# Performance work log

Measured on AMD Instinct MI355X. Metric: run time of the kernel, lower is better.

## Reference

```python
import jax, jax.numpy as jnp
import numpy as np

B, S, D, H = 8, 1024, 1024, 16
DH = D // H


def setup_inputs() -> dict:
    key = jax.random.key(0)
    ks = jax.random.split(key, 7)
    scale = 1.0 / np.sqrt(DH)
    return {
        "sequences": jax.random.normal(ks[0], (B, S, D), dtype=jnp.float32),
        "Wq": jax.random.uniform(ks[1], (H, DH, DH), jnp.float32, -scale, scale),
        "bq": jax.random.uniform(ks[2], (H, DH), jnp.float32, -scale, scale),
        "Wk": jax.random.uniform(ks[3], (H, DH, DH), jnp.float32, -scale, scale),
        "bk": jax.random.uniform(ks[4], (H, DH), jnp.float32, -scale, scale),
        "Wv": jax.random.uniform(ks[5], (H, DH, DH), jnp.float32, -scale, scale),
        "bv": jax.random.uniform(ks[6], (H, DH), jnp.float32, -scale, scale),
    }


def reference(sequences, Wq, bq, Wk, bk, Wv, bv):
    # split channels into heads: [B,S,H,DH]
    x = sequences.reshape(B, S, H, DH)
    # per-head linear maps (torch Linear: y = x @ W.T + b)
    q = jnp.einsum("bshd,hed->bshe", x, Wq) + bq  # [B,S,H,DH]
    k = jnp.einsum("bshd,hed->bshe", x, Wk) + bk
    v = jnp.einsum("bshd,hed->bshe", x, Wv) + bv
    scores = jnp.einsum("bshd,bthd->bhst", q, k) / jnp.sqrt(jnp.asarray(DH, x.dtype))
    attn = jax.nn.softmax(scores, axis=-1)  # [B,H,S,S]
    out = jnp.einsum("bhst,bthd->bshd", attn, v)  # [B,S,H,DH]
    return out.reshape(B, S, D)
```

## Files before the change

### kernel.cpp

```cpp
#include <hip/hip_runtime.h>
#include <hip/hip_bf16.h>


constexpr int NB = 8, NS = 1024, ND = 1024, NH = 16, NDH = 64;

typedef __bf16 bf16x8 __attribute__((ext_vector_type(8)));
typedef short bf16x4s __attribute__((ext_vector_type(4)));
typedef float f32x4 __attribute__((ext_vector_type(4)));

__device__ __forceinline__ f32x4 mfma16(bf16x8 a, bf16x8 b, f32x4 c) {
  return __builtin_amdgcn_mfma_f32_16x16x32_bf16(a, b, c, 0, 0, 0);
}

__device__ __forceinline__ f32x4 mfma16k16(bf16x4s a, bf16x4s b, f32x4 c) {
#if __has_builtin(__builtin_amdgcn_mfma_f32_16x16x16bf16_1k)
  return __builtin_amdgcn_mfma_f32_16x16x16bf16_1k(a, b, c, 0, 0, 0);
#else
  f32x4 d;
  asm("v_mfma_f32_16x16x16_bf16 %0, %1, %2, %3"
      : "=v"(d) : "v"(a), "v"(b), "v"(c));
  return d;
#endif
}

__device__ __forceinline__ float fast_exp2(float x) {
#if __has_builtin(__builtin_amdgcn_exp2f)
  return __builtin_amdgcn_exp2f(x);
#else
  return __builtin_exp2f(x);
#endif
}

__device__ __forceinline__ bf16x8 cvt2bf8(float4 lo, float4 hi) {
  bf16x8 r;
  r[0] = (__bf16)lo.x; r[1] = (__bf16)lo.y; r[2] = (__bf16)lo.z; r[3] = (__bf16)lo.w;
  r[4] = (__bf16)hi.x; r[5] = (__bf16)hi.y; r[6] = (__bf16)hi.z; r[7] = (__bf16)hi.w;
  return r;
}

__device__ __forceinline__ void gload16(const __hip_bfloat16* g, __hip_bfloat16* l) {
  __builtin_amdgcn_global_load_lds(
      (const __attribute__((address_space(1))) void*)g,
      (__attribute__((address_space(3))) void*)l, 16, 0, 0);
}

__device__ __forceinline__ unsigned pack_bf16(float hi, float lo) {
  unsigned uh = __builtin_bit_cast(unsigned, hi) + 0x8000u;
  unsigned ul = __builtin_bit_cast(unsigned, lo) + 0x8000u;
  return __builtin_amdgcn_perm(uh, ul, 0x07060302u);
}

__global__ __launch_bounds__(256) void qkv_proj_kernel(
    const float* __restrict__ x,
    const float* __restrict__ Wq, const float* __restrict__ bq,
    const float* __restrict__ Wk, const float* __restrict__ bk,
    const float* __restrict__ Wv, const float* __restrict__ bv,
    __hip_bfloat16* __restrict__ Qo, __hip_bfloat16* __restrict__ Ko,
    __hip_bfloat16* __restrict__ Vt) {
  __shared__ __align__(16) __hip_bfloat16 Wlds[3][NDH][72];
  const int tid = threadIdx.x;
  const int wave = tid >> 6, lane = tid & 63;
  const int m = lane & 15, quad = lane >> 4;
  const int h = blockIdx.x & (NH - 1);
  const int sblk = blockIdx.x >> 4;

  const float* Ws[3] = {Wq + h * 4096, Wk + h * 4096, Wv + h * 4096};
#pragma unroll
  for (int mt = 0; mt < 3; mt++) {
#pragma unroll
    for (int p = 0; p < 4; p++) {
      int idx = (p * 256 + tid) * 4;
      float4 v = *(const float4*)(Ws[mt] + idx);
      __align__(8) __hip_bfloat16 t4[4] = {
          __float2bfloat16(v.x), __float2bfloat16(v.y),
          __float2bfloat16(v.z), __float2bfloat16(v.w)};
      *(uint2*)&Wlds[mt][idx >> 6][idx & 63] = *(const uint2*)t4;
    }
  }
  __syncthreads();

  float bq4[4][4], bk4[4][4], bvv[4];
#pragma unroll
  for (int nt = 0; nt < 4; nt++) {
    float4 a = *(const float4*)(bq + h * 64 + nt * 16 + quad * 4);
    float4 c = *(const float4*)(bk + h * 64 + nt * 16 + quad * 4);
    bq4[nt][0] = a.x; bq4[nt][1] = a.y; bq4[nt][2] = a.z; bq4[nt][3] = a.w;
    bk4[nt][0] = c.x; bk4[nt][1] = c.y; bk4[nt][2] = c.z; bk4[nt][3] = c.w;
    bvv[nt] = bv[h * 64 + nt * 16 + m];
  }

  const int rowbase = sblk * 256 + wave * 64;
  bf16x8 Xf[4][2];
#pragma unroll
  for (int st = 0; st < 4; st++) {
    const float* xp = x + (size_t)(rowbase + st * 16 + m) * ND + h * NDH + quad * 8;
#pragma unroll
    for (int c = 0; c < 2; c++) {
      float4 lo = *(const float4*)(xp + c * 32);
      float4 hi = *(const float4*)(xp + c * 32 + 4);
      Xf[st][c] = cvt2bf8(lo, hi);
    }
  }

  const int b = rowbase >> 10;
  const int s0 = rowbase & 1023;
  const float qscale = 0.18033688011112042f;

#pragma unroll
  for (int mt = 0; mt < 3; mt++) {
#pragma unroll
    for (int nt = 0; nt < 4; nt++) {
      bf16x8 w0 = *(const bf16x8*)&Wlds[mt][nt * 16 + m][quad * 8];
      bf16x8 w1 = *(const bf16x8*)&Wlds[mt][nt * 16 + m][32 + quad * 8];
#pragma unroll
      for (int st = 0; st < 4; st++) {
        f32x4 acc = {0.f, 0.f, 0.f, 0.f};
        if (mt < 2) {
          acc = mfma16(w0, Xf[st][0], acc);
          acc = mfma16(w1, Xf[st][1], acc);
          const int srow = s0 + st * 16 + m;
          __align__(8) __hip_bfloat16 t4[4];
          if (mt == 0) {
#pragma unroll
            for (int r = 0; r < 4; r++)
              t4[r] = __float2bfloat16((acc[r] + bq4[nt][r]) * qscale);
            *(uint2*)(Qo + ((size_t)(b * NH + h) * NS + srow) * NDH +
                      nt * 16 + quad * 4) = *(const uint2*)t4;
          } else {
#pragma unroll
            for (int r = 0; r < 4; r++)
              t4[r] = __float2bfloat16(acc[r] + bk4[nt][r]);
            *(uint2*)(Ko + ((size_t)(b * NH + h) * NS + srow) * NDH +
                      nt * 16 + quad * 4) = *(const uint2*)t4;
          }
        } else {
          acc = mfma16(Xf[st][0], w0, acc);
          acc = mfma16(Xf[st][1], w1, acc);
          __align__(8) __hip_bfloat16 t4[4];
#pragma unroll
          for (int r = 0; r < 4; r++) t4[r] = __float2bfloat16(acc[r] + bvv[nt]);
          *(uint2*)(Vt + ((size_t)(b * NH + h) * NDH + nt * 16 + m) * NS + s0 +
                    st * 16 + quad * 4) = *(const uint2*)t4;
        }
      }
    }
  }
}

__global__ __launch_bounds__(256, 2) void attn_kernel(
    const __hip_bfloat16* __restrict__ Q,
    const __hip_bfloat16* __restrict__ K,
    const __hip_bfloat16* __restrict__ Vt,
    float* __restrict__ out) {
  __shared__ __align__(16) __hip_bfloat16 Kt[2][64][64];
  __shared__ __align__(16) __hip_bfloat16 Vl[2][64][64];

  const int tid = threadIdx.x;
  const int wave = tid >> 6, lane = tid & 63;
  const int m = lane & 15, quad = lane >> 4;

  const int xcd = blockIdx.x & 7;
  const int j = blockIdx.x >> 3;
  const int bh = xcd * 16 + (j & 15);
  const int qblk = j >> 4;
  const int qbase = qblk * 256 + wave * 64;

  const __hip_bfloat16* Qp = Q + (size_t)bh * NS * NDH;
  const __hip_bfloat16* Kp = K + (size_t)bh * NS * NDH;
  const __hip_bfloat16* Vp = Vt + (size_t)bh * NDH * NS;

  bf16x8 Bq[4][2];
#pragma unroll
  for (int g = 0; g < 4; g++)
#pragma unroll
    for (int c = 0; c < 2; c++)
      Bq[g][c] = *(const bf16x8*)(Qp + (size_t)(qbase + g * 16 + m) * NDH +
                                  c * 32 + quad * 8);

  f32x4 accO[4][4];
  f32x4 lsum[4];
#pragma unroll
  for (int g = 0; g < 4; g++) {
    lsum[g] = (f32x4){0.f, 0.f, 0.f, 0.f};
#pragma unroll
    for (int nt = 0; nt < 4; nt++) accO[g][nt] = (f32x4){0.f, 0.f, 0.f, 0.f};
  }
  const bf16x4s ones4 = {0x3F80, 0x3F80, 0x3F80, 0x3F80};

  const int r8 = lane >> 3;
  const int cs = (lane & 7) ^ r8;
  const int pc = quad ^ (m & 7);
  int voffs[4];
#pragma unroll
  for (int s = 0; s < 4; s++)
    voffs[s] = (((2 * s) | (quad >> 1)) ^ (m & 7)) * 8 + (quad & 1) * 4;

#define STAGE(buf, tb)                                                        \
  {                                                                           \
    _Pragma("unroll") for (int p = 0; p < 2; p++) {                           \
      const int row = wave * 16 + p * 8;                                      \
      gload16(Kp + (size_t)((tb) * 64 + row + r8) * NDH + cs * 8,             \
              &Kt[buf][row][0]);                                              \
      gload16(Vp + (size_t)(row + r8) * NS + (tb) * 64 + cs * 8,              \
              &Vl[buf][row][0]);                                              \
    }                                                                         \
  }

  STAGE(0, 0);

  for (int tb = 0; tb < NS / 64; tb++) {
    const int cur = tb & 1;
    __syncthreads();
    if (tb + 1 < NS / 64) STAGE(cur ^ 1, tb + 1);

    bf16x8 kf[4][2];
#pragma unroll
    for (int nt = 0; nt < 4; nt++) {
      kf[nt][0] = *(const bf16x8*)&Kt[cur][nt * 16 + m][pc * 8];
      kf[nt][1] = *(const bf16x8*)&Kt[cur][nt * 16 + m][(pc ^ 4) * 8];
    }
    bf16x4s vf[4][4];
#pragma unroll
    for (int nt = 0; nt < 4; nt++)
#pragma unroll
      for (int s = 0; s < 4; s++)
        vf[nt][s] = __builtin_bit_cast(
            bf16x4s, *(const uint2*)&Vl[cur][nt * 16 + m][voffs[s]]);

#pragma unroll
    for (int g = 0; g < 4; g++) {
      f32x4 sc[4];
#pragma unroll
      for (int s = 0; s < 4; s++) {
        f32x4 a = {0.f, 0.f, 0.f, 0.f};
        a = mfma16(kf[s][0], Bq[g][0], a);
        a = mfma16(kf[s][1], Bq[g][1], a);
        sc[s] = a;
      }
      bf16x4s Pa[4];
#pragma unroll
      for (int s = 0; s < 4; s++) {
        float e0 = fast_exp2(sc[s][0]);
        float e1 = fast_exp2(sc[s][1]);
        float e2 = fast_exp2(sc[s][2]);
        float e3 = fast_exp2(sc[s][3]);
        uint2 w;
        w.x = pack_bf16(e1, e0);
        w.y = pack_bf16(e3, e2);
        Pa[s] = __builtin_bit_cast(bf16x4s, w);
      }
#pragma unroll
      for (int s = 0; s < 4; s++) lsum[g] = mfma16k16(Pa[s], ones4, lsum[g]);
#pragma unroll
      for (int nt = 0; nt < 4; nt++)
#pragma unroll
        for (int s = 0; s < 4; s++)
          accO[g][nt] = mfma16k16(Pa[s], vf[nt][s], accO[g][nt]);
    }
  }
#undef STAGE

  const int b = bh >> 4, h = bh & (NH - 1);
#pragma unroll
  for (int g = 0; g < 4; g++) {
#pragma unroll
    for (int r = 0; r < 4; r++) {
      float inv = 1.0f / lsum[g][r];
      int srow = qbase + g * 16 + quad * 4 + r;
      float* op = out + (size_t)(b * NS + srow) * ND + h * NDH;
#pragma unroll
      for (int nt = 0; nt < 4; nt++) op[nt * 16 + m] = accO[g][nt][r] * inv;
    }
  }
}

extern "C" void kernel_launch(void* const* d_in, const int* in_sizes, int n_in,
                              void* d_out, int out_size, void* d_ws, size_t ws_size,
                              hipStream_t stream) {
  const float* x  = (const float*)d_in[0];
  const float* Wq = (const float*)d_in[1];
  const float* bq = (const float*)d_in[2];
  const float* Wk = (const float*)d_in[3];
  const float* bk = (const float*)d_in[4];
  const float* Wv = (const float*)d_in[5];
  const float* bv = (const float*)d_in[6];
  float* out = (float*)d_out;

  const size_t elems = (size_t)NB * NH * NS * NDH;
  __hip_bfloat16* Qw = (__hip_bfloat16*)d_ws;
  __hip_bfloat16* Kw = Qw + elems;
  __hip_bfloat16* Vw = Kw + elems;

  qkv_proj_kernel<<<512, 256, 0, stream>>>(x, Wq, bq, Wk, bk, Wv, bv, Qw, Kw, Vw);
  attn_kernel<<<512, 256, 0, stream>>>(Qw, Kw, Vw, out);
}
```

Measured before the change: 149.6 us.

## Halve query rows per attention block to raise occupancy and grid size

Each attention wave now handles 32 query rows instead of 64, and each block 128 instead of 256. The grid doubles to 1024 blocks and the launch bound rises to 4 blocks per CU. The inner loop is reordered so score MFMAs, exp and packing happen per key subtile, and V fragments are loaded per output subtile, which cuts live registers. In exchange, each K/V tile staged in shared memory is reused by half as many queries, so shared-memory and L2 traffic double, and barrier overhead per unit of MFMA work grows.

```diff
diff --git a/kernel.cpp b/kernel.cpp
--- a/kernel.cpp
+++ b/kernel.cpp
@@ -147,7 +147,7 @@
   }
 }
 
-__global__ __launch_bounds__(256, 2) void attn_kernel(
+__global__ __launch_bounds__(256, 4) void attn_kernel(
     const __hip_bfloat16* __restrict__ Q,
     const __hip_bfloat16* __restrict__ K,
     const __hip_bfloat16* __restrict__ Vt,
@@ -163,24 +163,24 @@
   const int j = blockIdx.x >> 3;
   const int bh = xcd * 16 + (j & 15);
   const int qblk = j >> 4;
-  const int qbase = qblk * 256 + wave * 64;
+  const int qbase = qblk * 128 + wave * 32;
 
   const __hip_bfloat16* Qp = Q + (size_t)bh * NS * NDH;
   const __hip_bfloat16* Kp = K + (size_t)bh * NS * NDH;
   const __hip_bfloat16* Vp = Vt + (size_t)bh * NDH * NS;
 
-  bf16x8 Bq[4][2];
-#pragma unroll
-  for (int g = 0; g < 4; g++)
+  bf16x8 Bq[2][2];
+#pragma unroll
+  for (int g = 0; g < 2; g++)
 #pragma unroll
     for (int c = 0; c < 2; c++)
       Bq[g][c] = *(const bf16x8*)(Qp + (size_t)(qbase + g * 16 + m) * NDH +
                                   c * 32 + quad * 8);
 
-  f32x4 accO[4][4];
-  f32x4 lsum[4];
-#pragma unroll
-  for (int g = 0; g < 4; g++) {
+  f32x4 accO[2][4];
+  f32x4 lsum[2];
+#pragma unroll
+  for (int g = 0; g < 2; g++) {
     lsum[g] = (f32x4){0.f, 0.f, 0.f, 0.f};
 #pragma unroll
     for (int nt = 0; nt < 4; nt++) accO[g][nt] = (f32x4){0.f, 0.f, 0.f, 0.f};
@@ -213,56 +213,45 @@
     __syncthreads();
     if (tb + 1 < NS / 64) STAGE(cur ^ 1, tb + 1);
 
-    bf16x8 kf[4][2];
+    bf16x4s Pa[2][4];
+#pragma unroll
+    for (int s = 0; s < 4; s++) {
+      bf16x8 k0 = *(const bf16x8*)&Kt[cur][s * 16 + m][pc * 8];
+      bf16x8 k1 = *(const bf16x8*)&Kt[cur][s * 16 + m][(pc ^ 4) * 8];
+#pragma unroll
+      for (int g = 0; g < 2; g++) {
+        f32x4 a = {0.f, 0.f, 0.f, 0.f};
+        a = mfma16(k0, Bq[g][0], a);
+        a = mfma16(k1, Bq[g][1], a);
+        uint2 w;
+        w.x = pack_bf16(fast_exp2(a[1]), fast_exp2(a[0]));
+        w.y = pack_bf16(fast_exp2(a[3]), fast_exp2(a[2]));
+        Pa[g][s] = __builtin_bit_cast(bf16x4s, w);
+      }
+    }
+#pragma unroll
+    for (int g = 0; g < 2; g++)
+#pragma unroll
+      for (int s = 0; s < 4; s++) lsum[g] = mfma16k16(Pa[g][s], ones4, lsum[g]);
 #pragma unroll
     for (int nt = 0; nt < 4; nt++) {
-      kf[nt][0] = *(const bf16x8*)&Kt[cur][nt * 16 + m][pc * 8];
-      kf[nt][1] = *(const bf16x8*)&Kt[cur][nt * 16 + m][(pc ^ 4) * 8];
-    }
-    bf16x4s vf[4][4];
-#pragma unroll
-    for (int nt = 0; nt < 4; nt++)
+      bf16x4s vf[4];
 #pragma unroll
       for (int s = 0; s < 4; s++)
-        vf[nt][s] = __builtin_bit_cast(
+        vf[s] = __builtin_bit_cast(
             bf16x4s, *(const uint2*)&Vl[cur][nt * 16 + m][voffs[s]]);
-
-#pragma unroll
-    for (int g = 0; g < 4; g++) {
-      f32x4 sc[4];
-#pragma unroll
-      for (int s = 0; s < 4; s++) {
-        f32x4 a = {0.f, 0.f, 0.f, 0.f};
-        a = mfma16(kf[s][0], Bq[g][0], a);
-        a = mfma16(kf[s][1], Bq[g][1], a);
-        sc[s] = a;
-      }
-      bf16x4s Pa[4];
-#pragma unroll
-      for (int s = 0; s < 4; s++) {
-        float e0 = fast_exp2(sc[s][0]);
-        float e1 = fast_exp2(sc[s][1]);
-        float e2 = fast_exp2(sc[s][2]);
-        float e3 = fast_exp2(sc[s][3]);
-        uint2 w;
-        w.x = pack_bf16(e1, e0);
-        w.y = pack_bf16(e3, e2);
-        Pa[s] = __builtin_bit_cast(bf16x4s, w);
-      }
-#pragma unroll
-      for (int s = 0; s < 4; s++) lsum[g] = mfma16k16(Pa[s], ones4, lsum[g]);
-#pragma unroll
-      for (int nt = 0; nt < 4; nt++)
+#pragma unroll
+      for (int g = 0; g < 2; g++)
 #pragma unroll
         for (int s = 0; s < 4; s++)
-          accO[g][nt] = mfma16k16(Pa[s], vf[nt][s], accO[g][nt]);
+          accO[g][nt] = mfma16k16(Pa[g][s], vf[s], accO[g][nt]);
     }
   }
 #undef STAGE
 
   const int b = bh >> 4, h = bh & (NH - 1);
 #pragma unroll
-  for (int g = 0; g < 4; g++) {
+  for (int g = 0; g < 2; g++) {
 #pragma unroll
     for (int r = 0; r < 4; r++) {
       float inv = 1.0f / lsum[g][r];
@@ -292,5 +281,5 @@
   __hip_bfloat16* Vw = Kw + elems;
 
   qkv_proj_kernel<<<512, 256, 0, stream>>>(x, Wq, bq, Wk, bk, Wv, bv, Qw, Kw, Vw);
-  attn_kernel<<<512, 256, 0, stream>>>(Qw, Kw, Vw, out);
-}
+  attn_kernel<<<1024, 256, 0, stream>>>(Qw, Kw, Vw, out);
+}
```

Measured after the change: 152.2 us. No clear change (+1.7%).

## Use 16x16x32 bf16 MFMA for PV and row-sum via permuted K rows

Applied to the files above, without the earlier changes.

Replaces the 16x16x16 MFMA used for P·V and the softmax row sum with the double-K 16x16x32 instruction. K rows are loaded in a permuted order with a new LDS swizzle, so the score output lanes line up with the 8-element A-operand layout that the wider MFMA expects. This halves the number of PV and row-sum MFMA instructions and allows wider LDS reads for V. The cost is more involved swizzle and index arithmetic, and correctness depends on the permutation matching on both the K side and the V side.

```diff
diff --git a/kernel.cpp b/kernel.cpp
--- a/kernel.cpp
+++ b/kernel.cpp
@@ -5,22 +5,10 @@
 constexpr int NB = 8, NS = 1024, ND = 1024, NH = 16, NDH = 64;
 
 typedef __bf16 bf16x8 __attribute__((ext_vector_type(8)));
-typedef short bf16x4s __attribute__((ext_vector_type(4)));
 typedef float f32x4 __attribute__((ext_vector_type(4)));
 
 __device__ __forceinline__ f32x4 mfma16(bf16x8 a, bf16x8 b, f32x4 c) {
   return __builtin_amdgcn_mfma_f32_16x16x32_bf16(a, b, c, 0, 0, 0);
-}
-
-__device__ __forceinline__ f32x4 mfma16k16(bf16x4s a, bf16x4s b, f32x4 c) {
-#if __has_builtin(__builtin_amdgcn_mfma_f32_16x16x16bf16_1k)
-  return __builtin_amdgcn_mfma_f32_16x16x16bf16_1k(a, b, c, 0, 0, 0);
-#else
-  f32x4 d;
-  asm("v_mfma_f32_16x16x16_bf16 %0, %1, %2, %3"
-      : "=v"(d) : "v"(a), "v"(b), "v"(c));
-  return d;
-#endif
 }
 
 __device__ __forceinline__ float fast_exp2(float x) {
@@ -173,9 +161,9 @@
 #pragma unroll
   for (int g = 0; g < 4; g++)
 #pragma unroll
-    for (int c = 0; c < 2; c++)
-      Bq[g][c] = *(const bf16x8*)(Qp + (size_t)(qbase + g * 16 + m) * NDH +
-                                  c * 32 + quad * 8);
+    for (int dh = 0; dh < 2; dh++)
+      Bq[g][dh] = *(const bf16x8*)(Qp + (size_t)(qbase + g * 16 + m) * NDH +
+                                   dh * 32 + quad * 8);
 
   f32x4 accO[4][4];
   f32x4 lsum[4];
@@ -185,24 +173,27 @@
 #pragma unroll
     for (int nt = 0; nt < 4; nt++) accO[g][nt] = (f32x4){0.f, 0.f, 0.f, 0.f};
   }
-  const bf16x4s ones4 = {0x3F80, 0x3F80, 0x3F80, 0x3F80};
+  bf16x8 ones8;
+#pragma unroll
+  for (int i = 0; i < 8; i++) ones8[i] = (__bf16)1.0f;
 
   const int r8 = lane >> 3;
-  const int cs = (lane & 7) ^ r8;
-  const int pc = quad ^ (m & 7);
-  int voffs[4];
-#pragma unroll
-  for (int s = 0; s < 4; s++)
-    voffs[s] = (((2 * s) | (quad >> 1)) ^ (m & 7)) * 8 + (quad & 1) * 4;
+  const int csV = (lane & 7) ^ r8;
+  const int csK0 = (lane & 7) ^ (r8 & 3);
+  const int krow = 8 * (m >> 2) + (m & 3);
+  const int fK = (m & 3) ^ (((m >> 2) & 1) << 2);
+  const int kc0 = ((quad ^ fK)) * 8;
+  const int vc0 = ((quad ^ (m & 7))) * 8;
 
 #define STAGE(buf, tb)                                                        \
   {                                                                           \
-    _Pragma("unroll") for (int p = 0; p < 2; p++) {                           \
-      const int row = wave * 16 + p * 8;                                      \
-      gload16(Kp + (size_t)((tb) * 64 + row + r8) * NDH + cs * 8,             \
-              &Kt[buf][row][0]);                                              \
-      gload16(Vp + (size_t)(row + r8) * NS + (tb) * 64 + cs * 8,              \
-              &Vl[buf][row][0]);                                              \
+    _Pragma("unroll") for (int p8 = 0; p8 < 2; p8++) {                        \
+      const int row0 = wave * 16 + p8 * 8;                                    \
+      gload16(Kp + (size_t)((tb) * 64 + row0 + r8) * NDH +                    \
+                  (csK0 ^ (p8 * 4)) * 8,                                      \
+              &Kt[buf][row0][0]);                                             \
+      gload16(Vp + (size_t)(row0 + r8) * NS + (tb) * 64 + csV * 8,            \
+              &Vl[buf][row0][0]);                                             \
     }                                                                         \
   }
 
@@ -213,49 +204,44 @@
     __syncthreads();
     if (tb + 1 < NS / 64) STAGE(cur ^ 1, tb + 1);
 
-    bf16x8 kf[4][2];
+    bf16x8 Pa[4][2];
+#pragma unroll
+    for (int c = 0; c < 2; c++) {
+      uint2 pw[4][2];
+#pragma unroll
+      for (int p = 0; p < 2; p++) {
+        const __hip_bfloat16* kr = &Kt[cur][c * 32 + 4 * p + krow][0];
+        bf16x8 k0 = *(const bf16x8*)(kr + kc0);
+        bf16x8 k1 = *(const bf16x8*)(kr + (kc0 ^ 32));
+#pragma unroll
+        for (int g = 0; g < 4; g++) {
+          f32x4 a = {0.f, 0.f, 0.f, 0.f};
+          a = mfma16(k0, Bq[g][0], a);
+          a = mfma16(k1, Bq[g][1], a);
+          pw[g][p].x = pack_bf16(fast_exp2(a[1]), fast_exp2(a[0]));
+          pw[g][p].y = pack_bf16(fast_exp2(a[3]), fast_exp2(a[2]));
+        }
+      }
+#pragma unroll
+      for (int g = 0; g < 4; g++) {
+        uint4 u = {pw[g][0].x, pw[g][0].y, pw[g][1].x, pw[g][1].y};
+        Pa[g][c] = __builtin_bit_cast(bf16x8, u);
+      }
+    }
+#pragma unroll
+    for (int g = 0; g < 4; g++)
+#pragma unroll
+      for (int c = 0; c < 2; c++) lsum[g] = mfma16(Pa[g][c], ones8, lsum[g]);
 #pragma unroll
     for (int nt = 0; nt < 4; nt++) {
-      kf[nt][0] = *(const bf16x8*)&Kt[cur][nt * 16 + m][pc * 8];
-      kf[nt][1] = *(const bf16x8*)&Kt[cur][nt * 16 + m][(pc ^ 4) * 8];
-    }
-    bf16x4s vf[4][4];
-#pragma unroll
-    for (int nt = 0; nt < 4; nt++)
-#pragma unroll
-      for (int s = 0; s < 4; s++)
-        vf[nt][s] = __builtin_bit_cast(
-            bf16x4s, *(const uint2*)&Vl[cur][nt * 16 + m][voffs[s]]);
-
-#pragma unroll
-    for (int g = 0; g < 4; g++) {
-      f32x4 sc[4];
-#pragma unroll
-      for (int s = 0; s < 4; s++) {
-        f32x4 a = {0.f, 0.f, 0.f, 0.f};
-        a = mfma16(kf[s][0], Bq[g][0], a);
-        a = mfma16(kf[s][1], Bq[g][1], a);
-        sc[s] = a;
-      }
-      bf16x4s Pa[4];
-#pragma unroll
-      for (int s = 0; s < 4; s++) {
-        float e0 = fast_exp2(sc[s][0]);
-        float e1 = fast_exp2(sc[s][1]);
-        float e2 = fast_exp2(sc[s][2]);
-        float e3 = fast_exp2(sc[s][3]);
-        uint2 w;
-        w.x = pack_bf16(e1, e0);
-        w.y = pack_bf16(e3, e2);
-        Pa[s] = __builtin_bit_cast(bf16x4s, w);
-      }
-#pragma unroll
-      for (int s = 0; s < 4; s++) lsum[g] = mfma16k16(Pa[s], ones4, lsum[g]);
-#pragma unroll
-      for (int nt = 0; nt < 4; nt++)
-#pragma unroll
-        for (int s = 0; s < 4; s++)
-          accO[g][nt] = mfma16k16(Pa[s], vf[nt][s], accO[g][nt]);
+      const __hip_bfloat16* vr = &Vl[cur][nt * 16 + m][0];
+      bf16x8 v0 = *(const bf16x8*)(vr + vc0);
+      bf16x8 v1 = *(const bf16x8*)(vr + (vc0 ^ 32));
+#pragma unroll
+      for (int g = 0; g < 4; g++) {
+        accO[g][nt] = mfma16(Pa[g][0], v0, accO[g][nt]);
+        accO[g][nt] = mfma16(Pa[g][1], v1, accO[g][nt]);
+      }
     }
   }
 #undef STAGE
```

Result: faster. 145.7 us (-2.6%).
